# Optimization experiments

Measured on AMD Instinct MI355X. Metric: run time of the kernel, lower is better.

The kernel has to match this reference:

```python
import jax, jax.numpy as jnp
import numpy as np

N_STREAMS = 4
HIDDEN = 1024
SINKHORN_ITERS = 20
TAU = 0.05
EPS = 1e-6
RMS_EPS = 1e-8


def rms_norm(x, weight):
    # x: [T, d] fp32
    rms = jnp.mean(x * x, axis=-1, keepdims=True)
    return x * jax.lax.rsqrt(rms + RMS_EPS) * weight


def sinkhorn_log(logits, n_iters=SINKHORN_ITERS, tau=TAU):
    # logits: [T, n, n] -> doubly-stochastic [T, n, n]
    Z = logits / tau
    u0 = jnp.zeros(Z.shape[:-1], Z.dtype)  # [T, n]
    v0 = jnp.zeros_like(u0)

    def body(i, uv):
        u, v = uv
        u = -jax.nn.logsumexp(Z + v[..., None, :], axis=-1)
        v = -jax.nn.logsumexp(Z + u[..., :, None], axis=-2)
        return (u, v)

    u, v = jax.lax.fori_loop(0, n_iters, body, (u0, v0))
    return jnp.exp(Z + u[..., :, None] + v[..., None, :])


def setup_inputs() -> dict:
    key = jax.random.key(0)
    ks = jax.random.split(key, 6)
    d = N_STREAMS * HIDDEN
    x_streams = jax.random.normal(ks[0], (4, 2048, N_STREAMS, HIDDEN), dtype=jnp.float32)
    scale = 1.0 / np.sqrt(d)
    return {
        "x_streams": x_streams,
        "rms_weight": jnp.ones((d,), jnp.float32),
        "W_pre": jax.random.normal(ks[1], (N_STREAMS, d), jnp.float32) * scale,
        "W_post": jax.random.normal(ks[2], (N_STREAMS, d), jnp.float32) * scale,
        "W_res": jax.random.normal(ks[3], (N_STREAMS * N_STREAMS, d), jnp.float32) * scale,
        "bias_pre": jnp.zeros((N_STREAMS,), jnp.float32),
        "bias_post": jnp.zeros((N_STREAMS,), jnp.float32),
        "bias_res": jnp.zeros((N_STREAMS * N_STREAMS,), jnp.float32),
        "alpha_pre": jnp.full((1,), 0.01, jnp.float32),
        "alpha_post": jnp.full((1,), 0.01, jnp.float32),
        "alpha_res": jnp.full((1,), 0.01, jnp.float32),
        "W_sub": jax.random.normal(ks[4], (HIDDEN, HIDDEN), jnp.float32) * (1.0 / np.sqrt(HIDDEN)),
    }


def reference(x_streams, rms_weight, W_pre, W_post, W_res, bias_pre, bias_post,
              bias_res, alpha_pre, alpha_post, alpha_res, W_sub):
    B, S, n, C = x_streams.shape
    d = n * C
    x_flat = x_streams.reshape(B * S, d).astype(jnp.float32)
    x_norm = rms_norm(x_flat, rms_weight)

    H_pre = jax.nn.sigmoid(alpha_pre * (x_norm @ W_pre.T) + bias_pre)        # [T, n]
    H_post = 2.0 * jax.nn.sigmoid(alpha_post * (x_norm @ W_post.T) + bias_post)
    H_res = sinkhorn_log((alpha_res * (x_norm @ W_res.T) + bias_res).reshape(B * S, n, n))

    H_pre = H_pre.reshape(B, S, n)
    H_post = H_post.reshape(B, S, n)
    H_res = H_res.reshape(B, S, n, n)

    H_pre_w = H_pre / (jnp.sum(H_pre, axis=-1, keepdims=True) + EPS)
    H_post_w = H_post / (jnp.sum(H_post, axis=-1, keepdims=True) + EPS)

    # pre-aggregate streams -> single stream
    x_layer = jnp.einsum('bsnc,bsn->bsc', x_streams, H_pre_w)
    # sublayer: bias-free linear
    y = x_layer @ W_sub.T                                                    # [B, S, C]
    # broadcast sublayer output back to streams
    y_expanded = H_post_w[..., None] * y[:, :, None, :]                      # [B, S, n, C]
    # doubly-stochastic residual stream mixing
    x_mixed = jnp.einsum('bsic,bsoi->bsoc', x_streams, H_res)
    return x_mixed + y_expanded
```

## Files before the change

### kernel.cpp

```cpp
#include <hip/hip_runtime.h>

#define NTOK 8192
#define D 4096
#define CH 1024

typedef __attribute__((ext_vector_type(8))) short short8v;
typedef __attribute__((ext_vector_type(4))) float float4v;
typedef __attribute__((ext_vector_type(4))) unsigned short ushort4v;

static __device__ __forceinline__ unsigned short f2bf(float f) {
  unsigned int u = __float_as_uint(f);
  u += 0x7fff + ((u >> 16) & 1);
  return (unsigned short)(u >> 16);
}

static __device__ __forceinline__ void async_cp16(const void* g, void* l) {
  __builtin_amdgcn_global_load_lds((__attribute__((address_space(1))) void*)g,
                                   (__attribute__((address_space(3))) void*)l,
                                   16, 0, 0);
}

__global__ __launch_bounds__(256) void prep_wsub(const float* __restrict__ Wsub,
                                                 unsigned short* __restrict__ Wb) {
  int i = blockIdx.x * 256 + threadIdx.x;
  float4 v = ((const float4*)Wsub)[i];
  ushort4v o;
  o.x = f2bf(v.x); o.y = f2bf(v.y); o.z = f2bf(v.z); o.w = f2bf(v.w);
  ((ushort4v*)Wb)[i] = o;
}

__global__ __launch_bounds__(256) void gates_kernel(
    const float* __restrict__ x, const float* __restrict__ rms_w,
    const float* __restrict__ Wpre, const float* __restrict__ Wpost,
    const float* __restrict__ Wres, const float* __restrict__ bpre,
    const float* __restrict__ bpost, const float* __restrict__ bres,
    const float* __restrict__ apre, const float* __restrict__ apost,
    const float* __restrict__ ares, float* __restrict__ gates_out,
    unsigned short* __restrict__ xlayer) {
  __shared__ float xbuf[2][8][256];
  __shared__ float logits_lds[8][24];
  __shared__ float sq_lds[8];
  __shared__ float s_lds[8];
  __shared__ float hpre_lds[8][4];

  const int tid = threadIdx.x;
  const int lane = tid & 63;
  const int w = tid >> 6;
  const int tok0 = blockIdx.x * 8;

  const float* Wp[6];
#pragma unroll
  for (int g = 0; g < 6; ++g) {
    int gg = w * 6 + g;
    Wp[g] = (gg < 4) ? (Wpre + gg * D)
          : (gg < 8) ? (Wpost + (gg - 4) * D)
                     : (Wres + (gg - 8) * D);
  }

  float acc[6][8];
#pragma unroll
  for (int g = 0; g < 6; ++g)
#pragma unroll
    for (int t = 0; t < 8; ++t) acc[g][t] = 0.f;
  float sq0 = 0.f, sq1 = 0.f;

  async_cp16(x + (size_t)(tok0 + 2 * w) * D + lane * 4, (void*)&xbuf[0][2 * w][0]);
  async_cp16(x + (size_t)(tok0 + 2 * w + 1) * D + lane * 4, (void*)&xbuf[0][2 * w + 1][0]);
  __syncthreads();

  for (int chk = 0; chk < 16; ++chk) {
    const int cb = chk * 256;
    const int cur = chk & 1;
    if (chk < 15) {
      const int nb = cb + 256;
      async_cp16(x + (size_t)(tok0 + 2 * w) * D + nb + lane * 4,
                 (void*)&xbuf[cur ^ 1][2 * w][0]);
      async_cp16(x + (size_t)(tok0 + 2 * w + 1) * D + nb + lane * 4,
                 (void*)&xbuf[cur ^ 1][2 * w + 1][0]);
    }
    float4 w4[6];
#pragma unroll
    for (int g = 0; g < 6; ++g) w4[g] = *(const float4*)(Wp[g] + cb + lane * 4);
    float4 r4 = *(const float4*)(rms_w + cb + lane * 4);
#pragma unroll
    for (int t = 0; t < 8; ++t) {
      float4 xv = *(const float4*)(&xbuf[cur][t][lane * 4]);
      float ss = xv.x * xv.x + xv.y * xv.y + xv.z * xv.z + xv.w * xv.w;
      if ((t >> 1) == w) { if (t & 1) sq1 += ss; else sq0 += ss; }
      float4 xr;
      xr.x = xv.x * r4.x; xr.y = xv.y * r4.y; xr.z = xv.z * r4.z; xr.w = xv.w * r4.w;
#pragma unroll
      for (int g = 0; g < 6; ++g)
        acc[g][t] += xr.x * w4[g].x + xr.y * w4[g].y + xr.z * w4[g].z + xr.w * w4[g].w;
    }
    __syncthreads();
  }

#pragma unroll
  for (int g = 0; g < 6; ++g)
#pragma unroll
    for (int t = 0; t < 8; ++t) {
      float v = acc[g][t];
      for (int off = 32; off > 0; off >>= 1) v += __shfl_xor(v, off, 64);
      if (lane == 0) logits_lds[t][w * 6 + g] = v;
    }
  {
    float v0 = sq0, v1 = sq1;
    for (int off = 32; off > 0; off >>= 1) {
      v0 += __shfl_xor(v0, off, 64);
      v1 += __shfl_xor(v1, off, 64);
    }
    if (lane == 0) { sq_lds[w * 2] = v0; sq_lds[w * 2 + 1] = v1; }
  }
  __syncthreads();

  if (tid < 8) {
    const int t = tid;
    float s = rsqrtf(sq_lds[t] * (1.0f / 4096.0f) + 1e-8f);
    s_lds[t] = s;
    float a_pre = apre[0], a_post = apost[0];

    float hp[4];
    float sum_p = 1e-6f;
#pragma unroll
    for (int i = 0; i < 4; ++i) {
      float z = a_pre * (s * logits_lds[t][i]) + bpre[i];
      hp[i] = 1.0f / (1.0f + __expf(-z));
      sum_p += hp[i];
    }
    float inv_p = 1.0f / sum_p;
#pragma unroll
    for (int i = 0; i < 4; ++i) hpre_lds[t][i] = hp[i] * inv_p;

    float* go = gates_out + (size_t)(tok0 + t) * 20;
    float hq[4];
    float sum_q = 1e-6f;
#pragma unroll
    for (int i = 0; i < 4; ++i) {
      float z = a_post * (s * logits_lds[t][4 + i]) + bpost[i];
      hq[i] = 2.0f / (1.0f + __expf(-z));
      sum_q += hq[i];
    }
    float inv_q = 1.0f / sum_q;
#pragma unroll
    for (int i = 0; i < 4; ++i) go[i] = hq[i] * inv_q;
  }
  __syncthreads();

#pragma unroll
  for (int t = 0; t < 8; ++t) {
    float h0 = hpre_lds[t][0], h1 = hpre_lds[t][1];
    float h2 = hpre_lds[t][2], h3 = hpre_lds[t][3];
    const size_t base = (size_t)(tok0 + t) * D;
    float4 x0 = *(const float4*)(x + base + 0 * CH + tid * 4);
    float4 x1 = *(const float4*)(x + base + 1 * CH + tid * 4);
    float4 x2 = *(const float4*)(x + base + 2 * CH + tid * 4);
    float4 x3 = *(const float4*)(x + base + 3 * CH + tid * 4);
    ushort4v o;
    o.x = f2bf(h0 * x0.x + h1 * x1.x + h2 * x2.x + h3 * x3.x);
    o.y = f2bf(h0 * x0.y + h1 * x1.y + h2 * x2.y + h3 * x3.y);
    o.z = f2bf(h0 * x0.z + h1 * x1.z + h2 * x2.z + h3 * x3.z);
    o.w = f2bf(h0 * x0.w + h1 * x1.w + h2 * x2.w + h3 * x3.w);
    *(ushort4v*)(xlayer + (size_t)(tok0 + t) * CH + tid * 4) = o;
  }

  if (tid < 32) {
    const int t = tid >> 2;
    const int r = tid & 3;
    const float s = s_lds[t];
    const float a_res = ares[0];
    float Zrow[4], Zcol[4];
#pragma unroll
    for (int j = 0; j < 4; ++j) {
      Zrow[j] = (a_res * (s * logits_lds[t][8 + r * 4 + j]) + bres[r * 4 + j]) * 20.0f;
      Zcol[j] = (a_res * (s * logits_lds[t][8 + j * 4 + r]) + bres[j * 4 + r]) * 20.0f;
    }
    float u = 0.f, v = 0.f;
    const int base = t << 2;
    for (int it = 0; it < 20; ++it) {
      float v0 = __shfl(v, base + 0, 64), v1 = __shfl(v, base + 1, 64);
      float v2 = __shfl(v, base + 2, 64), v3 = __shfl(v, base + 3, 64);
      float a0 = Zrow[0] + v0, a1 = Zrow[1] + v1, a2 = Zrow[2] + v2, a3 = Zrow[3] + v3;
      float m = fmaxf(fmaxf(a0, a1), fmaxf(a2, a3));
      float sm = __expf(a0 - m) + __expf(a1 - m) + __expf(a2 - m) + __expf(a3 - m);
      u = -(m + __logf(sm));
      float u0 = __shfl(u, base + 0, 64), u1 = __shfl(u, base + 1, 64);
      float u2 = __shfl(u, base + 2, 64), u3 = __shfl(u, base + 3, 64);
      float b0 = Zcol[0] + u0, b1 = Zcol[1] + u1, b2 = Zcol[2] + u2, b3 = Zcol[3] + u3;
      float m2 = fmaxf(fmaxf(b0, b1), fmaxf(b2, b3));
      float sm2 = __expf(b0 - m2) + __expf(b1 - m2) + __expf(b2 - m2) + __expf(b3 - m2);
      v = -(m2 + __logf(sm2));
    }
    float v0 = __shfl(v, base + 0, 64), v1 = __shfl(v, base + 1, 64);
    float v2 = __shfl(v, base + 2, 64), v3 = __shfl(v, base + 3, 64);
    float* go = gates_out + (size_t)(tok0 + t) * 20;
    go[4 + r * 4 + 0] = __expf(Zrow[0] + u + v0);
    go[4 + r * 4 + 1] = __expf(Zrow[1] + u + v1);
    go[4 + r * 4 + 2] = __expf(Zrow[2] + u + v2);
    go[4 + r * 4 + 3] = __expf(Zrow[3] + u + v3);
  }
}

__global__ __launch_bounds__(256) void gemm_epi(
    const unsigned short* __restrict__ A,
    const unsigned short* __restrict__ B,
    const float* __restrict__ x,
    const float* __restrict__ gates,
    float* __restrict__ out) {
  __shared__ __align__(16) char lds_raw[128 * 132 * 4];
  __shared__ float gsm[128 * 20];
  unsigned short* stg = (unsigned short*)lds_raw;
  float* ybuf = (float*)lds_raw;

  const int tid = threadIdx.x;
  const int lane = tid & 63;
  const int w = tid >> 6;
  const int n0 = blockIdx.x * 128;
  const int m0 = blockIdx.y * 128;

  for (int i = tid; i < 128 * 20; i += 256) gsm[i] = gates[(size_t)m0 * 20 + i];

  float4v accf[4][4];
#pragma unroll
  for (int mi = 0; mi < 4; ++mi)
#pragma unroll
    for (int ni = 0; ni < 4; ++ni) {
      accf[mi][ni].x = 0.f; accf[mi][ni].y = 0.f;
      accf[mi][ni].z = 0.f; accf[mi][ni].w = 0.f;
    }

  const int wm = (w >> 1) * 64;
  const int wn = (w & 1) * 64;
  const int srow = lane >> 3;
  const int sslot = lane & 7;

#define STAGE(KT, BUF)                                                        \
  {                                                                           \
    const int k0s = (KT) * 64;                                                \
    unsigned short* As = stg + (BUF) * 8192;                                  \
    unsigned short* Bs = stg + 16384 + (BUF) * 8192;                          \
    _Pragma("unroll")                                                         \
    for (int i = 0; i < 4; ++i) {                                             \
      int chunk = w * 4 + i;                                                  \
      int row = chunk * 8 + srow;                                             \
      int qg = sslot ^ (row & 7);                                             \
      async_cp16(A + (size_t)(m0 + row) * 1024 + k0s + qg * 8,                \
                 (void*)(As + chunk * 512));                                  \
      async_cp16(B + (size_t)(n0 + row) * 1024 + k0s + qg * 8,                \
                 (void*)(Bs + chunk * 512));                                  \
    }                                                                         \
  }

  STAGE(0, 0);
  __syncthreads();

  for (int kt = 0; kt < 16; ++kt) {
    const int cur = kt & 1;
    if (kt < 15) STAGE(kt + 1, cur ^ 1);
    const unsigned short* As = stg + cur * 8192;
    const unsigned short* Bs = stg + 16384 + cur * 8192;
#pragma unroll
    for (int kk = 0; kk < 2; ++kk) {
      short8v a[4], b[4];
#pragma unroll
      for (int mi = 0; mi < 4; ++mi) {
        int row = wm + mi * 16 + (lane & 15);
        int q = (kk * 4 + (lane >> 4)) ^ (row & 7);
        a[mi] = *(const short8v*)(As + row * 64 + q * 8);
      }
#pragma unroll
      for (int ni = 0; ni < 4; ++ni) {
        int row = wn + ni * 16 + (lane & 15);
        int q = (kk * 4 + (lane >> 4)) ^ (row & 7);
        b[ni] = *(const short8v*)(Bs + row * 64 + q * 8);
      }
#pragma unroll
      for (int mi = 0; mi < 4; ++mi)
#pragma unroll
        for (int ni = 0; ni < 4; ++ni)
          accf[mi][ni] = __builtin_amdgcn_mfma_f32_16x16x32_bf16(
              a[mi], b[ni], accf[mi][ni], 0, 0, 0);
    }
    __syncthreads();
  }

#pragma unroll
  for (int mi = 0; mi < 4; ++mi)
#pragma unroll
    for (int ni = 0; ni < 4; ++ni)
#pragma unroll
      for (int r = 0; r < 4; ++r) {
        int row = wm + mi * 16 + (lane >> 4) * 4 + r;
        int col = wn + ni * 16 + (lane & 15);
        ybuf[row * 132 + col] = accf[mi][ni][r];
      }
  __syncthreads();

#pragma unroll 4
  for (int i = 0; i < 16; ++i) {
    int idx = i * 256 + tid;
    int tl = idx >> 5;
    int c4 = idx & 31;
    const size_t t = (size_t)(m0 + tl);
    const float* gp = gsm + tl * 20;
    float4 y4 = *(const float4*)&ybuf[tl * 132 + c4 * 4];
    const size_t xb = t * 4096 + n0 + c4 * 4;
    float4 x0 = *(const float4*)(x + xb);
    float4 x1 = *(const float4*)(x + xb + 1024);
    float4 x2 = *(const float4*)(x + xb + 2048);
    float4 x3 = *(const float4*)(x + xb + 3072);
#pragma unroll
    for (int o = 0; o < 4; ++o) {
      float h0 = gp[4 + o * 4 + 0], h1 = gp[4 + o * 4 + 1];
      float h2 = gp[4 + o * 4 + 2], h3 = gp[4 + o * 4 + 3];
      float hp = gp[o];
      float4 rr;
      rr.x = x0.x * h0 + x1.x * h1 + x2.x * h2 + x3.x * h3 + hp * y4.x;
      rr.y = x0.y * h0 + x1.y * h1 + x2.y * h2 + x3.y * h3 + hp * y4.y;
      rr.z = x0.z * h0 + x1.z * h1 + x2.z * h2 + x3.z * h3 + hp * y4.z;
      rr.w = x0.w * h0 + x1.w * h1 + x2.w * h2 + x3.w * h3 + hp * y4.w;
      *(float4*)(out + t * 4096 + (size_t)o * 1024 + n0 + c4 * 4) = rr;
    }
  }
}

extern "C" void kernel_launch(void* const* d_in, const int* in_sizes, int n_in,
                              void* d_out, int out_size, void* d_ws, size_t ws_size,
                              hipStream_t stream) {
  const float* x     = (const float*)d_in[0];
  const float* rms_w = (const float*)d_in[1];
  const float* Wpre  = (const float*)d_in[2];
  const float* Wpost = (const float*)d_in[3];
  const float* Wres  = (const float*)d_in[4];
  const float* bpre  = (const float*)d_in[5];
  const float* bpost = (const float*)d_in[6];
  const float* bres  = (const float*)d_in[7];
  const float* apre  = (const float*)d_in[8];
  const float* apost = (const float*)d_in[9];
  const float* ares  = (const float*)d_in[10];
  const float* Wsub  = (const float*)d_in[11];
  float* out = (float*)d_out;

  char* ws = (char*)d_ws;
  float* gates           = (float*)ws;
  unsigned short* Wb     = (unsigned short*)(ws + (1 << 20));
  unsigned short* xlayer = (unsigned short*)(ws + (4 << 20));

  prep_wsub<<<1024, 256, 0, stream>>>(Wsub, Wb);
  gates_kernel<<<1024, 256, 0, stream>>>(x, rms_w, Wpre, Wpost, Wres, bpre,
                                         bpost, bres, apre, apost, ares,
                                         gates, xlayer);
  gemm_epi<<<dim3(8, 64), 256, 0, stream>>>(xlayer, Wb, x, gates, out);
}
```

Measured before the change: 424.6 us.

## Fold Wsub bf16 conversion into gates kernel and double its block size

Removes the separate prep_wsub launch by having each gates_kernel block convert a 1024-element slice of W_sub to bf16. The gates kernel grows from 256 to 512 threads (8 waves), so each wave handles 3 gate rows and one token's x tile instead of 6 rows and two tokens. The intent is to save one kernel launch and raise per-block parallelism and latency hiding. The cost is fewer resident blocks per CU and more weight loads per block, since each wave now reads its own gate rows.

```diff
diff --git a/kernel.cpp b/kernel.cpp
--- a/kernel.cpp
+++ b/kernel.cpp
@@ -20,22 +20,14 @@
                                    16, 0, 0);
 }
 
-__global__ __launch_bounds__(256) void prep_wsub(const float* __restrict__ Wsub,
-                                                 unsigned short* __restrict__ Wb) {
-  int i = blockIdx.x * 256 + threadIdx.x;
-  float4 v = ((const float4*)Wsub)[i];
-  ushort4v o;
-  o.x = f2bf(v.x); o.y = f2bf(v.y); o.z = f2bf(v.z); o.w = f2bf(v.w);
-  ((ushort4v*)Wb)[i] = o;
-}
-
-__global__ __launch_bounds__(256) void gates_kernel(
+__global__ __launch_bounds__(512) void gates_kernel(
     const float* __restrict__ x, const float* __restrict__ rms_w,
     const float* __restrict__ Wpre, const float* __restrict__ Wpost,
     const float* __restrict__ Wres, const float* __restrict__ bpre,
     const float* __restrict__ bpost, const float* __restrict__ bres,
     const float* __restrict__ apre, const float* __restrict__ apost,
-    const float* __restrict__ ares, float* __restrict__ gates_out,
+    const float* __restrict__ ares, const float* __restrict__ Wsub,
+    unsigned short* __restrict__ Wb, float* __restrict__ gates_out,
     unsigned short* __restrict__ xlayer) {
   __shared__ float xbuf[2][8][256];
   __shared__ float logits_lds[8][24];
@@ -48,69 +40,68 @@
   const int w = tid >> 6;
   const int tok0 = blockIdx.x * 8;
 
-  const float* Wp[6];
-#pragma unroll
-  for (int g = 0; g < 6; ++g) {
-    int gg = w * 6 + g;
+  {
+    int i = blockIdx.x * 1024 + tid * 2;
+    float2 v = *(const float2*)(Wsub + i);
+    unsigned int packed = (unsigned int)f2bf(v.x) | ((unsigned int)f2bf(v.y) << 16);
+    *(unsigned int*)(Wb + i) = packed;
+  }
+
+  const float* Wp[3];
+#pragma unroll
+  for (int g = 0; g < 3; ++g) {
+    int gg = w * 3 + g;
     Wp[g] = (gg < 4) ? (Wpre + gg * D)
           : (gg < 8) ? (Wpost + (gg - 4) * D)
                      : (Wres + (gg - 8) * D);
   }
 
-  float acc[6][8];
-#pragma unroll
-  for (int g = 0; g < 6; ++g)
+  float acc[3][8];
+#pragma unroll
+  for (int g = 0; g < 3; ++g)
 #pragma unroll
     for (int t = 0; t < 8; ++t) acc[g][t] = 0.f;
-  float sq0 = 0.f, sq1 = 0.f;
-
-  async_cp16(x + (size_t)(tok0 + 2 * w) * D + lane * 4, (void*)&xbuf[0][2 * w][0]);
-  async_cp16(x + (size_t)(tok0 + 2 * w + 1) * D + lane * 4, (void*)&xbuf[0][2 * w + 1][0]);
+  float sq = 0.f;
+
+  async_cp16(x + (size_t)(tok0 + w) * D + lane * 4, (void*)&xbuf[0][w][0]);
   __syncthreads();
 
   for (int chk = 0; chk < 16; ++chk) {
     const int cb = chk * 256;
     const int cur = chk & 1;
-    if (chk < 15) {
-      const int nb = cb + 256;
-      async_cp16(x + (size_t)(tok0 + 2 * w) * D + nb + lane * 4,
-                 (void*)&xbuf[cur ^ 1][2 * w][0]);
-      async_cp16(x + (size_t)(tok0 + 2 * w + 1) * D + nb + lane * 4,
-                 (void*)&xbuf[cur ^ 1][2 * w + 1][0]);
-    }
-    float4 w4[6];
-#pragma unroll
-    for (int g = 0; g < 6; ++g) w4[g] = *(const float4*)(Wp[g] + cb + lane * 4);
+    if (chk < 15)
+      async_cp16(x + (size_t)(tok0 + w) * D + cb + 256 + lane * 4,
+                 (void*)&xbuf[cur ^ 1][w][0]);
+    float4 w4[3];
+#pragma unroll
+    for (int g = 0; g < 3; ++g) w4[g] = *(const float4*)(Wp[g] + cb + lane * 4);
     float4 r4 = *(const float4*)(rms_w + cb + lane * 4);
 #pragma unroll
     for (int t = 0; t < 8; ++t) {
       float4 xv = *(const float4*)(&xbuf[cur][t][lane * 4]);
-      float ss = xv.x * xv.x + xv.y * xv.y + xv.z * xv.z + xv.w * xv.w;
-      if ((t >> 1) == w) { if (t & 1) sq1 += ss; else sq0 += ss; }
+      if (t == w)
+        sq += xv.x * xv.x + xv.y * xv.y + xv.z * xv.z + xv.w * xv.w;
       float4 xr;
       xr.x = xv.x * r4.x; xr.y = xv.y * r4.y; xr.z = xv.z * r4.z; xr.w = xv.w * r4.w;
 #pragma unroll
-      for (int g = 0; g < 6; ++g)
+      for (int g = 0; g < 3; ++g)
         acc[g][t] += xr.x * w4[g].x + xr.y * w4[g].y + xr.z * w4[g].z + xr.w * w4[g].w;
     }
     __syncthreads();
   }
 
 #pragma unroll
-  for (int g = 0; g < 6; ++g)
+  for (int g = 0; g < 3; ++g)
 #pragma unroll
     for (int t = 0; t < 8; ++t) {
       float v = acc[g][t];
       for (int off = 32; off > 0; off >>= 1) v += __shfl_xor(v, off, 64);
-      if (lane == 0) logits_lds[t][w * 6 + g] = v;
+      if (lane == 0) logits_lds[t][w * 3 + g] = v;
     }
   {
-    float v0 = sq0, v1 = sq1;
-    for (int off = 32; off > 0; off >>= 1) {
-      v0 += __shfl_xor(v0, off, 64);
-      v1 += __shfl_xor(v1, off, 64);
-    }
-    if (lane == 0) { sq_lds[w * 2] = v0; sq_lds[w * 2 + 1] = v1; }
+    float v = sq;
+    for (int off = 32; off > 0; off >>= 1) v += __shfl_xor(v, off, 64);
+    if (lane == 0) sq_lds[w] = v;
   }
   __syncthreads();
 
@@ -147,21 +138,26 @@
   }
   __syncthreads();
 
-#pragma unroll
-  for (int t = 0; t < 8; ++t) {
-    float h0 = hpre_lds[t][0], h1 = hpre_lds[t][1];
-    float h2 = hpre_lds[t][2], h3 = hpre_lds[t][3];
-    const size_t base = (size_t)(tok0 + t) * D;
-    float4 x0 = *(const float4*)(x + base + 0 * CH + tid * 4);
-    float4 x1 = *(const float4*)(x + base + 1 * CH + tid * 4);
-    float4 x2 = *(const float4*)(x + base + 2 * CH + tid * 4);
-    float4 x3 = *(const float4*)(x + base + 3 * CH + tid * 4);
-    ushort4v o;
-    o.x = f2bf(h0 * x0.x + h1 * x1.x + h2 * x2.x + h3 * x3.x);
-    o.y = f2bf(h0 * x0.y + h1 * x1.y + h2 * x2.y + h3 * x3.y);
-    o.z = f2bf(h0 * x0.z + h1 * x1.z + h2 * x2.z + h3 * x3.z);
-    o.w = f2bf(h0 * x0.w + h1 * x1.w + h2 * x2.w + h3 * x3.w);
-    *(ushort4v*)(xlayer + (size_t)(tok0 + t) * CH + tid * 4) = o;
+  {
+    const int col = (tid & 255) * 4;
+    const int half = tid >> 8;
+#pragma unroll
+    for (int r = 0; r < 4; ++r) {
+      const int t = r * 2 + half;
+      float h0 = hpre_lds[t][0], h1 = hpre_lds[t][1];
+      float h2 = hpre_lds[t][2], h3 = hpre_lds[t][3];
+      const size_t base = (size_t)(tok0 + t) * D;
+      float4 x0 = *(const float4*)(x + base + 0 * CH + col);
+      float4 x1 = *(const float4*)(x + base + 1 * CH + col);
+      float4 x2 = *(const float4*)(x + base + 2 * CH + col);
+      float4 x3 = *(const float4*)(x + base + 3 * CH + col);
+      ushort4v o;
+      o.x = f2bf(h0 * x0.x + h1 * x1.x + h2 * x2.x + h3 * x3.x);
+      o.y = f2bf(h0 * x0.y + h1 * x1.y + h2 * x2.y + h3 * x3.y);
+      o.z = f2bf(h0 * x0.z + h1 * x1.z + h2 * x2.z + h3 * x3.z);
+      o.w = f2bf(h0 * x0.w + h1 * x1.w + h2 * x2.w + h3 * x3.w);
+      *(ushort4v*)(xlayer + (size_t)(tok0 + t) * CH + col) = o;
+    }
   }
 
   if (tid < 32) {
@@ -346,9 +342,8 @@
   unsigned short* Wb     = (unsigned short*)(ws + (1 << 20));
   unsigned short* xlayer = (unsigned short*)(ws + (4 << 20));
 
-  prep_wsub<<<1024, 256, 0, stream>>>(Wsub, Wb);
-  gates_kernel<<<1024, 256, 0, stream>>>(x, rms_w, Wpre, Wpost, Wres, bpre,
+  gates_kernel<<<1024, 512, 0, stream>>>(x, rms_w, Wpre, Wpost, Wres, bpre,
                                          bpost, bres, apre, apost, ares,
-                                         gates, xlayer);
+                                         Wsub, Wb, gates, xlayer);
   gemm_epi<<<dim3(8, 64), 256, 0, stream>>>(xlayer, Wb, x, gates, out);
 }
```

After: 381.7 us. -10.1%, faster.
